# Kernel tuning notes

Measured on AMD Instinct MI355X. Metric: run time of the kernel, lower is better.

Reference implementation:

```python
import jax, jax.numpy as jnp
import numpy as np

MARGIN = 0.3
HARD_FACTOR = 0.0
EPS = 1e-6


def setup_inputs() -> dict:
    key = jax.random.key(0)
    k1, k2 = jax.random.split(key)
    inputs = jax.random.normal(k1, (4096, 256), dtype=jnp.float32)
    targets = jax.random.randint(k2, (4096,), 0, 512, dtype=jnp.int64)
    return {"inputs": inputs, "targets": targets}


def reference(inputs, targets):
    n = inputs.shape[0]
    half = n // 2
    # L2-normalize features (matches normalize(): x / (||x|| + 1e-6))
    x = inputs / (jnp.linalg.norm(inputs, axis=-1, keepdims=True) + EPS)
    # pairwise euclidean distances, clamped at 1e-6 before sqrt
    sq = jnp.sum(x * x, axis=1)                      # (n,)
    dist = sq[:, None] + sq[None, :] - 2.0 * (x @ x.T)  # (n, n)
    dist = jnp.sqrt(jnp.clip(dist, EPS))
    # same-identity mask
    mask = targets[:, None] == targets[None, :]      # (n, n) bool
    # rows in the first half mine over columns [half:n], rows in the
    # second half mine over columns [0:half] -> gather the opposite half
    first = (jnp.arange(n) < half)[:, None]          # (n, 1)
    d_o = jnp.where(first, dist[:, half:], dist[:, :half])  # (n, half)
    m_o = jnp.where(first, mask[:, half:], mask[:, :half])  # (n, half) bool
    pos_any = jnp.any(m_o, axis=1)
    neg_any = jnp.any(~m_o, axis=1)
    dist_ap = jnp.where(pos_any,
                        jnp.max(jnp.where(m_o, d_o, -jnp.inf), axis=1),
                        0.0)
    dist_an = jnp.where(neg_any,
                        jnp.min(jnp.where(m_o, jnp.inf, d_o), axis=1),
                        1.0)
    dist_ap = dist_ap * (1.0 + HARD_FACTOR)
    dist_an = dist_an * (1.0 - HARD_FACTOR)
    # MarginRankingLoss(margin)(dist_an, dist_ap, y=1) =
    #   mean(relu(-(dist_an - dist_ap) + margin))
    loss = jnp.mean(jax.nn.relu(dist_ap - dist_an + MARGIN))
    return loss
```

## Files before the change

kernel.cpp:

```cpp
#include <hip/hip_runtime.h>
#include <math.h>

#define N 4096
#define D 256
#define HALF 2048
#define MARGIN 0.3f

#define BM 64
#define NTB (HALF/BM)

typedef __attribute__((ext_vector_type(8))) short bf16x8;
typedef __attribute__((ext_vector_type(4))) float f32x4;

__device__ __forceinline__ unsigned short bf16_rne(float x) {
    unsigned int u = __float_as_uint(x);
    return (unsigned short)((u + 0x7fffu + ((u >> 16) & 1u)) >> 16);
}

__global__ __launch_bounds__(256) void k_norm(const float* __restrict__ in,
                                              unsigned short* __restrict__ xnb,
                                              float* __restrict__ sq,
                                              int* __restrict__ ap,
                                              int* __restrict__ an,
                                              float* __restrict__ acc_sum,
                                              int* __restrict__ acc_cnt) {
    const int wave = threadIdx.x >> 6, lane = threadIdx.x & 63;
    const int row = blockIdx.x * 4 + wave;
    float4 v = *(const float4*)&in[(size_t)row * D + lane * 4];
    float s = v.x * v.x + v.y * v.y + v.z * v.z + v.w * v.w;
#pragma unroll
    for (int o = 1; o < 64; o <<= 1) s += __shfl_xor(s, o, 64);
    float nrm = sqrtf(s);
    float inv = 1.0f / (nrm + 1e-6f);
    ushort4 h;
    h.x = bf16_rne(v.x * inv);
    h.y = bf16_rne(v.y * inv);
    h.z = bf16_rne(v.z * inv);
    h.w = bf16_rne(v.w * inv);
    *(ushort4*)&xnb[(size_t)row * D + lane * 4] = h;
    if (lane == 0) {
        float q = nrm * inv;
        sq[row] = q * q;
        ap[row] = 0;
        an[row] = 0x7f800000;
    }
    if (blockIdx.x == 0 && threadIdx.x == 0) {
        *acc_sum = 0.f;
        *acc_cnt = 0;
    }
}

__global__ __launch_bounds__(256) void k_tile(const unsigned short* __restrict__ xnb,
                                              const float* __restrict__ sq,
                                              const int* __restrict__ tg,
                                              int* __restrict__ ap,
                                              int* __restrict__ an) {
    __shared__ int sra[BM], srn[BM], sca[BM], scn[BM];

    const int bi = blockIdx.y, bj = blockIdx.x;
    const int I0 = bi * BM;
    const int J0 = bj * BM;
    const int tid = threadIdx.x;
    const int wave = tid >> 6, lane = tid & 63;
    const int wm = wave >> 1, wn = wave & 1;
    const int lrow = lane & 15, lquad = lane >> 4;

    const unsigned short* A0 = xnb + (size_t)(I0 + wm * 32 + lrow) * D + lquad * 8;
    const unsigned short* A1 = A0 + (size_t)16 * D;
    const unsigned short* B0 = xnb + (size_t)(HALF + J0 + wn * 32 + lrow) * D + lquad * 8;
    const unsigned short* B1 = B0 + (size_t)16 * D;

    f32x4 acc[2][2];
#pragma unroll
    for (int a = 0; a < 2; ++a)
#pragma unroll
        for (int b = 0; b < 2; ++b) acc[a][b] = (f32x4){0.f, 0.f, 0.f, 0.f};

#pragma unroll
    for (int k0 = 0; k0 < D; k0 += 32) {
        bf16x8 a0 = *(const bf16x8*)(A0 + k0);
        bf16x8 a1 = *(const bf16x8*)(A1 + k0);
        bf16x8 b0 = *(const bf16x8*)(B0 + k0);
        bf16x8 b1 = *(const bf16x8*)(B1 + k0);
        acc[0][0] = __builtin_amdgcn_mfma_f32_16x16x32_bf16(a0, b0, acc[0][0], 0, 0, 0);
        acc[0][1] = __builtin_amdgcn_mfma_f32_16x16x32_bf16(a0, b1, acc[0][1], 0, 0, 0);
        acc[1][0] = __builtin_amdgcn_mfma_f32_16x16x32_bf16(a1, b0, acc[1][0], 0, 0, 0);
        acc[1][1] = __builtin_amdgcn_mfma_f32_16x16x32_bf16(a1, b1, acc[1][1], 0, 0, 0);
    }

    float sqi[2][4], sqj[2];
    int tgi[2][4], tgj[2];
#pragma unroll
    for (int mi = 0; mi < 2; ++mi)
#pragma unroll
        for (int r = 0; r < 4; ++r) {
            int lr = wm * 32 + mi * 16 + lquad * 4 + r;
            sqi[mi][r] = sq[I0 + lr];
            tgi[mi][r] = tg[I0 + lr];
        }
#pragma unroll
    for (int nj = 0; nj < 2; ++nj) {
        int lc = wn * 32 + nj * 16 + lrow;
        sqj[nj] = sq[HALF + J0 + lc];
        tgj[nj] = tg[HALF + J0 + lc];
    }

    const float INF = __int_as_float(0x7f800000);
    float rap[2][4], ran[2][4], capv[2], canv[2];
#pragma unroll
    for (int mi = 0; mi < 2; ++mi)
#pragma unroll
        for (int r = 0; r < 4; ++r) { rap[mi][r] = 0.f; ran[mi][r] = INF; }
#pragma unroll
    for (int nj = 0; nj < 2; ++nj) { capv[nj] = 0.f; canv[nj] = INF; }

#pragma unroll
    for (int mi = 0; mi < 2; ++mi)
#pragma unroll
        for (int nj = 0; nj < 2; ++nj)
#pragma unroll
            for (int r = 0; r < 4; ++r) {
                float d2 = sqi[mi][r] + sqj[nj] - 2.0f * acc[mi][nj][r];
                float d = sqrtf(fmaxf(d2, 1e-6f));
                if (tgi[mi][r] == tgj[nj]) {
                    rap[mi][r] = fmaxf(rap[mi][r], d);
                    capv[nj] = fmaxf(capv[nj], d);
                } else {
                    ran[mi][r] = fminf(ran[mi][r], d);
                    canv[nj] = fminf(canv[nj], d);
                }
            }

#pragma unroll
    for (int mi = 0; mi < 2; ++mi)
#pragma unroll
        for (int r = 0; r < 4; ++r)
#pragma unroll
            for (int o = 1; o < 16; o <<= 1) {
                rap[mi][r] = fmaxf(rap[mi][r], __shfl_xor(rap[mi][r], o, 64));
                ran[mi][r] = fminf(ran[mi][r], __shfl_xor(ran[mi][r], o, 64));
            }
#pragma unroll
    for (int nj = 0; nj < 2; ++nj)
#pragma unroll
        for (int o = 16; o < 64; o <<= 1) {
            capv[nj] = fmaxf(capv[nj], __shfl_xor(capv[nj], o, 64));
            canv[nj] = fminf(canv[nj], __shfl_xor(canv[nj], o, 64));
        }

    if (tid < BM) { sra[tid] = 0; srn[tid] = 0x7f800000;
                    sca[tid] = 0; scn[tid] = 0x7f800000; }
    __syncthreads();
    if (lrow == 0) {
#pragma unroll
        for (int mi = 0; mi < 2; ++mi)
#pragma unroll
            for (int r = 0; r < 4; ++r) {
                int lr = wm * 32 + mi * 16 + lquad * 4 + r;
                atomicMax(&sra[lr], __float_as_int(rap[mi][r]));
                atomicMin(&srn[lr], __float_as_int(ran[mi][r]));
            }
    }
    if (lquad == 0) {
#pragma unroll
        for (int nj = 0; nj < 2; ++nj) {
            int lc = wn * 32 + nj * 16 + lrow;
            atomicMax(&sca[lc], __float_as_int(capv[nj]));
            atomicMin(&scn[lc], __float_as_int(canv[nj]));
        }
    }
    __syncthreads();
    if (tid < BM) {
        atomicMax(&ap[I0 + tid], sra[tid]);
        atomicMin(&an[I0 + tid], srn[tid]);
        atomicMax(&ap[HALF + J0 + tid], sca[tid]);
        atomicMin(&an[HALF + J0 + tid], scn[tid]);
    }
}

__global__ __launch_bounds__(64) void k_reduce(const int* __restrict__ ap,
                                               const int* __restrict__ an,
                                               float* __restrict__ acc_sum,
                                               int* __restrict__ acc_cnt,
                                               float* __restrict__ out) {
    const int lane = threadIdx.x;
    const int gid = blockIdx.x * 64 + lane;
    float dap = __int_as_float(ap[gid]);
    int anb = an[gid];
    float dan = (anb == 0x7f800000) ? 1.0f : __int_as_float(anb);
    float v = dap - dan + MARGIN;
    float s = (v > 0.f) ? v : 0.f;
#pragma unroll
    for (int o = 1; o < 64; o <<= 1) s += __shfl_xor(s, o, 64);
    if (lane == 0) {
        atomicAdd(acc_sum, s);
        __threadfence();
        int old = atomicAdd(acc_cnt, 1);
        if (old == 63) {
            float tot = atomicAdd(acc_sum, 0.0f);
            out[0] = tot / (float)N;
        }
    }
}

extern "C" void kernel_launch(void* const* d_in, const int* in_sizes, int n_in,
                              void* d_out, int out_size, void* d_ws, size_t ws_size,
                              hipStream_t stream) {
    const float* in = (const float*)d_in[0];
    const int* tg = (const int*)d_in[1];
    float* out = (float*)d_out;

    unsigned short* xnb = (unsigned short*)d_ws;
    float* sq = (float*)(xnb + (size_t)N * D);
    int* ap = (int*)(sq + N);
    int* an = ap + N;
    float* acc_sum = (float*)(an + N);
    int* acc_cnt = (int*)(acc_sum + 1);

    k_norm<<<N / 4, 256, 0, stream>>>(in, xnb, sq, ap, an, acc_sum, acc_cnt);
    k_tile<<<dim3(NTB, NTB), 256, 0, stream>>>(xnb, sq, tg, ap, an);
    k_reduce<<<64, 64, 0, stream>>>(ap, an, acc_sum, acc_cnt, out);
}
```

Baseline: 80.24 us.

## Stage A/B tiles through double-buffered LDS instead of direct global loads

The MFMA tile kernel now loads each 64x32 bf16 slice of A and B cooperatively into padded shared memory, double-buffered across the K loop, and waves read their fragments from LDS. Before, each wave fetched its fragments straight from global memory and the two waves sharing a row or column block duplicated those loads. Staging is meant to cut redundant global/L2 traffic and overlap the next slice's load with the current MFMAs. In exchange it adds a barrier per K step, LDS traffic, and an occupancy hint of 4 blocks per SM in launch_bounds.

```diff
diff --git a/kernel.cpp b/kernel.cpp
--- a/kernel.cpp
+++ b/kernel.cpp
@@ -7,7 +7,9 @@
 #define MARGIN 0.3f
 
 #define BM 64
+#define BK 32
 #define NTB (HALF/BM)
+#define LDB 40
 
 typedef __attribute__((ext_vector_type(8))) short bf16x8;
 typedef __attribute__((ext_vector_type(4))) float f32x4;
@@ -50,11 +52,13 @@
     }
 }
 
-__global__ __launch_bounds__(256) void k_tile(const unsigned short* __restrict__ xnb,
-                                              const float* __restrict__ sq,
-                                              const int* __restrict__ tg,
-                                              int* __restrict__ ap,
-                                              int* __restrict__ an) {
+__global__ __launch_bounds__(256, 4) void k_tile(const unsigned short* __restrict__ xnb,
+                                                 const float* __restrict__ sq,
+                                                 const int* __restrict__ tg,
+                                                 int* __restrict__ ap,
+                                                 int* __restrict__ an) {
+    __shared__ unsigned short As[2][BM * LDB];
+    __shared__ unsigned short Bs[2][BM * LDB];
     __shared__ int sra[BM], srn[BM], sca[BM], scn[BM];
 
     const int bi = blockIdx.y, bj = blockIdx.x;
@@ -65,10 +69,13 @@
     const int wm = wave >> 1, wn = wave & 1;
     const int lrow = lane & 15, lquad = lane >> 4;
 
-    const unsigned short* A0 = xnb + (size_t)(I0 + wm * 32 + lrow) * D + lquad * 8;
-    const unsigned short* A1 = A0 + (size_t)16 * D;
-    const unsigned short* B0 = xnb + (size_t)(HALF + J0 + wn * 32 + lrow) * D + lquad * 8;
-    const unsigned short* B1 = B0 + (size_t)16 * D;
+    const int srow = tid >> 2, schunk = (tid & 3) * 8;
+    const unsigned short* Agp = xnb + (size_t)(I0 + srow) * D + schunk;
+    const unsigned short* Bgp = xnb + (size_t)(HALF + J0 + srow) * D + schunk;
+    unsigned short* Asp0 = &As[0][srow * LDB + schunk];
+    unsigned short* Bsp0 = &Bs[0][srow * LDB + schunk];
+    unsigned short* Asp1 = &As[1][srow * LDB + schunk];
+    unsigned short* Bsp1 = &Bs[1][srow * LDB + schunk];
 
     f32x4 acc[2][2];
 #pragma unroll
@@ -76,16 +83,40 @@
 #pragma unroll
         for (int b = 0; b < 2; ++b) acc[a][b] = (f32x4){0.f, 0.f, 0.f, 0.f};
 
-#pragma unroll
-    for (int k0 = 0; k0 < D; k0 += 32) {
-        bf16x8 a0 = *(const bf16x8*)(A0 + k0);
-        bf16x8 a1 = *(const bf16x8*)(A1 + k0);
-        bf16x8 b0 = *(const bf16x8*)(B0 + k0);
-        bf16x8 b1 = *(const bf16x8*)(B1 + k0);
-        acc[0][0] = __builtin_amdgcn_mfma_f32_16x16x32_bf16(a0, b0, acc[0][0], 0, 0, 0);
-        acc[0][1] = __builtin_amdgcn_mfma_f32_16x16x32_bf16(a0, b1, acc[0][1], 0, 0, 0);
-        acc[1][0] = __builtin_amdgcn_mfma_f32_16x16x32_bf16(a1, b0, acc[1][0], 0, 0, 0);
-        acc[1][1] = __builtin_amdgcn_mfma_f32_16x16x32_bf16(a1, b1, acc[1][1], 0, 0, 0);
+    {
+        uint4 a0 = *(const uint4*)Agp;
+        uint4 b0 = *(const uint4*)Bgp;
+        *(uint4*)Asp0 = a0;
+        *(uint4*)Bsp0 = b0;
+    }
+    __syncthreads();
+
+#pragma unroll
+    for (int s = 0; s < D / BK; ++s) {
+        const int p = s & 1;
+        uint4 an_, bn_;
+        if (s < D / BK - 1) {
+            an_ = *(const uint4*)(Agp + (s + 1) * BK);
+            bn_ = *(const uint4*)(Bgp + (s + 1) * BK);
+        }
+        bf16x8 af[2], bfr[2];
+#pragma unroll
+        for (int mi = 0; mi < 2; ++mi)
+            af[mi] = *(const bf16x8*)&As[p][(wm * 32 + mi * 16 + lrow) * LDB + lquad * 8];
+#pragma unroll
+        for (int nj = 0; nj < 2; ++nj)
+            bfr[nj] = *(const bf16x8*)&Bs[p][(wn * 32 + nj * 16 + lrow) * LDB + lquad * 8];
+#pragma unroll
+        for (int mi = 0; mi < 2; ++mi)
+#pragma unroll
+            for (int nj = 0; nj < 2; ++nj)
+                acc[mi][nj] = __builtin_amdgcn_mfma_f32_16x16x32_bf16(
+                    af[mi], bfr[nj], acc[mi][nj], 0, 0, 0);
+        if (s < D / BK - 1) {
+            if (p) { *(uint4*)Asp0 = an_; *(uint4*)Bsp0 = bn_; }
+            else   { *(uint4*)Asp1 = an_; *(uint4*)Bsp1 = bn_; }
+            __syncthreads();
+        }
     }
 
     float sqi[2][4], sqj[2];
```

Measured after the change: 72.93 us. 9.1% less time.
